# Kernel optimization log

Hardware: AMD Instinct MI355X
Metric: run time of the kernel (lower is better)

## Reference

```python
import jax, jax.numpy as jnp
import numpy as np

N, D, C, S = 100000, 512, 4096, 50000


def setup_inputs() -> dict:
    key = jax.random.key(0)
    k1, k2 = jax.random.split(key)
    X = jax.random.normal(k1, (N, D), dtype=jnp.float32)
    codebook_sum = jax.random.normal(k2, (C, D), dtype=jnp.float32)
    prompt_mask = jnp.arange(N) < S  # first S rows are support (True), rest are queries
    return {"X": X, "codebook_sum": codebook_sum, "prompt_mask": prompt_mask, "num_support": S}


def reference(X, codebook_sum, prompt_mask, num_support):
    # num_support is a static Python int (replaces torch.nonzero(prompt_mask) dynamic split)
    s = num_support
    support = X[:s]                                   # [S, D] support (prompt_mask==True)
    query = X[s:]                                     # [Q, D] queries (prompt_mask==False)
    # dense similarity matmul + top-1 nearest-codebook search + gather
    cos_sim = jnp.einsum('sd,cd->sc', support, codebook_sum)  # [S, C]
    top_idx = jnp.argmax(cos_sim, axis=1)             # [S]
    code_n = codebook_sum[top_idx]                    # [S, D] gathered nearest codes
    # mean-pooled prototypes broadcast over queries
    proto = jnp.mean(support, axis=0)                 # [D]
    proto_code = jnp.mean(code_n, axis=0)             # [D]
    # euclidean distances to each prototype
    query_score = jnp.sqrt(jnp.sum((query - proto) ** 2, axis=1))        # [Q]
    query_score_code = jnp.sqrt(jnp.sum((query - proto_code) ** 2, axis=1))  # [Q]
    return (query_score + query_score_code) / 2
```

## Files before the change

### kernel.cpp

```cpp
#include <hip/hip_runtime.h>
#include <hip/hip_bf16.h>

#define NTOT 100000
#define DIM  512
#define CB   4096
#define SSUP 50000
#define NQ   (NTOT - SSUP)

#define MTILES 391
#define MPAD   (MTILES * 128)
#define NTILES 32
#define NWG    (MTILES * NTILES)
#define CPX    (NWG / 8)

typedef __bf16 bf16x8 __attribute__((ext_vector_type(8)));
typedef __bf16 bf16x4 __attribute__((ext_vector_type(4)));
typedef float  f32x4  __attribute__((ext_vector_type(4)));

#define OFF_CBBF   0
#define OFF_XB     4194304
#define OFF_PV     55443456
#define OFF_PI     61849600
#define OFF_PSUM   68255744
#define OFF_PCSUM  68257792
#define OFF_HIST   68259840
#define OFF_TIDX   68276224
#define WS_NEED    (68276224 + 200000)
#define ZERO_BYTES (2048 + 2048 + 16384)

#define F_OFF_PSUM   4194304
#define F_OFF_PCSUM  4196352
#define F_OFF_HIST   4198400
#define F_OFF_TIDX   4214784

__device__ __forceinline__ void load_lds16(const void* g, void* l) {
    __builtin_amdgcn_global_load_lds(
        (const __attribute__((address_space(1))) void*)g,
        (__attribute__((address_space(3))) void*)l, 16, 0, 0);
}

#define BARRIER() __builtin_amdgcn_s_barrier()
#define VMC(N)    asm volatile("s_waitcnt vmcnt(" #N ")" ::: "memory")

__global__ void k_convert(const float* __restrict__ src, __bf16* __restrict__ dst) {
    int i = (blockIdx.x * 256 + threadIdx.x) * 4;
    float4 v = *(const float4*)(src + i);
    bf16x4 o;
    o[0] = (__bf16)v.x; o[1] = (__bf16)v.y; o[2] = (__bf16)v.z; o[3] = (__bf16)v.w;
    *(bf16x4*)(dst + i) = o;
}

__global__ __launch_bounds__(256)
void k_conv_psum(const float* __restrict__ X, __bf16* __restrict__ Xb,
                 float* __restrict__ protoSum)
{
    __shared__ float red[4][512];
    const int tid  = threadIdx.x;
    const int c8   = (tid & 63) * 8;
    const int rsub = tid >> 6;
    const size_t rbase = (size_t)blockIdx.x * 128 + rsub;

    float acc[8];
    #pragma unroll
    for (int j = 0; j < 8; ++j) acc[j] = 0.f;

    for (int r = 0; r < 128; r += 4) {
        const size_t row = rbase + r;
        const float* p = X + row * DIM + c8;
        float4 v0 = *(const float4*)p;
        float4 v1 = *(const float4*)(p + 4);
        bf16x8 o;
        o[0] = (__bf16)v0.x; o[1] = (__bf16)v0.y; o[2] = (__bf16)v0.z; o[3] = (__bf16)v0.w;
        o[4] = (__bf16)v1.x; o[5] = (__bf16)v1.y; o[6] = (__bf16)v1.z; o[7] = (__bf16)v1.w;
        *(bf16x8*)(Xb + row * DIM + c8) = o;
        if (row < SSUP) {
            acc[0] += v0.x; acc[1] += v0.y; acc[2] += v0.z; acc[3] += v0.w;
            acc[4] += v1.x; acc[5] += v1.y; acc[6] += v1.z; acc[7] += v1.w;
        }
    }
    #pragma unroll
    for (int j = 0; j < 8; ++j) red[rsub][c8 + j] = acc[j];
    __syncthreads();
    if (rsub == 0) {
        #pragma unroll
        for (int j = 0; j < 8; ++j)
            atomicAdd(&protoSum[c8 + j],
                      red[0][c8 + j] + red[1][c8 + j] + red[2][c8 + j] + red[3][c8 + j]);
    }
}


template<int MH, int NH>
__device__ __forceinline__ void mfma_quad_dummy() {}

__global__ __launch_bounds__(256, 2)
void k_gemm128(const __bf16* __restrict__ Xb, const __bf16* __restrict__ cbb,
               float* __restrict__ pv, int* __restrict__ pi)
{
    __shared__ __align__(16) char lds[65536];
    __shared__ float sv[128][2];
    __shared__ int   si[128][2];

    const int tid  = threadIdx.x;
    const int lane = tid & 63;
    const int wid  = tid >> 6;
    const int wm   = wid >> 1;
    const int wn   = wid & 1;
    const int l15  = lane & 15;
    const int q    = lane >> 4;

    const int lin = blockIdx.y * NTILES + blockIdx.x;
    const int swz = (lin & 7) * CPX + (lin >> 3);
    const int mt  = swz >> 5;
    const int nt  = swz & 31;
    const size_t r0  = (size_t)mt * 128;
    const size_t c0g = (size_t)nt * 128;

    const int off0 = l15 * 128 + ((q)     ^ (l15 & 7)) * 16;
    const int off1 = l15 * 128 + ((4 + q) ^ (l15 & 7)) * 16;

    const int ck0 = tid, ck1 = 256 + tid;
    const int rw0 = ck0 >> 3, rw1 = ck1 >> 3;
    const int sc0 = (ck0 & 7) ^ (rw0 & 7);
    const int sc1 = (ck1 & 7) ^ (rw1 & 7);
    const __bf16* pA0 = Xb  + (r0  + rw0) * DIM + sc0 * 8;
    const __bf16* pA1 = Xb  + (r0  + rw1) * DIM + sc1 * 8;
    const __bf16* pB0 = cbb + (c0g + rw0) * DIM + sc0 * 8;
    const __bf16* pB1 = cbb + (c0g + rw1) * DIM + sc1 * 8;
    const int d0 = ck0 * 16, d1 = ck1 * 16;
    const size_t HROW = (size_t)64 * DIM;

    f32x4 acc[4][4];
    #pragma unroll
    for (int i = 0; i < 4; ++i)
        #pragma unroll
        for (int j = 0; j < 4; ++j)
            acc[i][j] = (f32x4){0.f, 0.f, 0.f, 0.f};

    auto STAGE = [&](int bufo, int kt) {
        const int ko = kt * 64;
        char* lb = lds + bufo;
        load_lds16(pA0 + ko,        lb + d0);
        load_lds16(pA1 + ko,        lb + d1);
        load_lds16(pA0 + HROW + ko, lb + 8192 + d0);
        load_lds16(pA1 + HROW + ko, lb + 8192 + d1);
        load_lds16(pB0 + ko,        lb + 16384 + d0);
        load_lds16(pB1 + ko,        lb + 16384 + d1);
        load_lds16(pB0 + HROW + ko, lb + 24576 + d0);
        load_lds16(pB1 + HROW + ko, lb + 24576 + d1);
    };

    auto COMPUTE = [&](int bufo) {
        const char* ap = lds + bufo + wm * 8192;
        const char* bp = lds + bufo + 16384 + wn * 8192;
        bf16x8 a[4][2], b[4][2];
        #pragma unroll
        for (int m = 0; m < 4; ++m) {
            a[m][0] = *(const bf16x8*)(ap + m * 2048 + off0);
            a[m][1] = *(const bf16x8*)(ap + m * 2048 + off1);
        }
        #pragma unroll
        for (int n = 0; n < 4; ++n) {
            b[n][0] = *(const bf16x8*)(bp + n * 2048 + off0);
            b[n][1] = *(const bf16x8*)(bp + n * 2048 + off1);
        }
        __builtin_amdgcn_s_setprio(1);
        #pragma unroll
        for (int m = 0; m < 4; ++m)
            #pragma unroll
            for (int n = 0; n < 4; ++n)
                #pragma unroll
                for (int ks = 0; ks < 2; ++ks)
                    acc[m][n] = __builtin_amdgcn_mfma_f32_16x16x32_bf16(
                        a[m][ks], b[n][ks], acc[m][n], 0, 0, 0);
        __builtin_amdgcn_s_setprio(0);
    };

    STAGE(0, 0);
    STAGE(32768, 1);
    VMC(8);
    BARRIER();

    #pragma unroll
    for (int t = 0; t < 6; t += 2) {
        COMPUTE(0);
        BARRIER();
        STAGE(0, t + 2);
        VMC(8);
        BARRIER();
        COMPUTE(32768);
        BARRIER();
        STAGE(32768, t + 3);
        VMC(8);
        BARRIER();
    }

    COMPUTE(0);
    BARRIER();
    VMC(0);
    BARRIER();
    COMPUTE(32768);

    #pragma unroll
    for (int fm = 0; fm < 4; ++fm) {
        #pragma unroll
        for (int reg = 0; reg < 4; ++reg) {
            float v = -3.0e38f; int idx = 0;
            #pragma unroll
            for (int fn = 0; fn < 4; ++fn) {
                float x = acc[fm][fn][reg];
                int   c = (int)c0g + wn * 64 + fn * 16 + l15;
                if (x > v) { v = x; idx = c; }
            }
            #pragma unroll
            for (int off = 1; off < 16; off <<= 1) {
                float ov = __shfl_xor(v, off, 64);
                int   oi = __shfl_xor(idx, off, 64);
                if (ov > v) { v = ov; idx = oi; }
            }
            if (l15 == 0) {
                int rl = wm * 64 + fm * 16 + q * 4 + reg;
                sv[rl][wn] = v;
                si[rl][wn] = idx;
            }
        }
    }
    __syncthreads();
    if (tid < 128) {
        float v0 = sv[tid][0], v1 = sv[tid][1];
        size_t r = r0 + tid;
        pv[r * 32 + nt] = fmaxf(v0, v1);
        pi[r * 32 + nt] = (v1 > v0) ? si[tid][1] : si[tid][0];
    }
}

__global__ __launch_bounds__(256)
void k_reduce_hist(const float* __restrict__ pv, const int* __restrict__ pi,
                   int* __restrict__ hist) {
    __shared__ int lh[CB];
    const int tid = threadIdx.x;
    for (int i = tid; i < CB; i += 256) lh[i] = 0;
    __syncthreads();
    const int r = blockIdx.x * 256 + tid;
    if (r < SSUP) {
        float v = -3.0e38f; int idx = 0;
        #pragma unroll 8
        for (int j = 0; j < 32; ++j) {
            float x = pv[(size_t)r * 32 + j];
            if (x > v) { v = x; idx = pi[(size_t)r * 32 + j]; }
        }
        atomicAdd(&lh[idx], 1);
    }
    __syncthreads();
    for (int i = tid; i < CB; i += 256) {
        int v = lh[i];
        if (v) atomicAdd(&hist[i], v);
    }
}

__global__ void k_proto_sum(const float* __restrict__ X, float* __restrict__ protoSum) {
    const int d = threadIdx.x;
    const int r0 = blockIdx.x * 500;
    float acc = 0.f;
    for (int r = r0; r < r0 + 500; ++r)
        acc += X[(size_t)r * DIM + d];
    atomicAdd(&protoSum[d], acc);
}

__global__ __launch_bounds__(256, 2)
void k_gemm_argmax(const float* __restrict__ X, const __bf16* __restrict__ cbb,
                   int* __restrict__ top_idx)
{
    __shared__ float redv[64][2];
    __shared__ int   redi[64][2];

    const int tid  = threadIdx.x;
    const int wave = tid >> 6;
    const int lane = tid & 63;
    const int wm   = wave >> 1;
    const int wn   = wave & 1;
    const int l15  = lane & 15;
    const int q    = lane >> 4;
    const int r0   = blockIdx.x * 64;

    bf16x8 aflat[2][16];
    #pragma unroll
    for (int tm = 0; tm < 2; ++tm) {
        const int r = r0 + wm * 32 + tm * 16 + l15;
        const bool valid = (r < SSUP);
        const float* xr = X + (size_t)r * DIM + q * 8;
        #pragma unroll
        for (int kt = 0; kt < 16; ++kt) {
            float4 v0, v1;
            if (valid) {
                v0 = *(const float4*)(xr + kt * 32);
                v1 = *(const float4*)(xr + kt * 32 + 4);
            } else {
                v0 = make_float4(0.f, 0.f, 0.f, 0.f);
                v1 = v0;
            }
            bf16x8 f;
            f[0] = (__bf16)v0.x; f[1] = (__bf16)v0.y; f[2] = (__bf16)v0.z; f[3] = (__bf16)v0.w;
            f[4] = (__bf16)v1.x; f[5] = (__bf16)v1.y; f[6] = (__bf16)v1.z; f[7] = (__bf16)v1.w;
            aflat[tm][kt] = f;
        }
    }

    float mx[8];
    int   mi[8];
    #pragma unroll
    for (int i = 0; i < 8; ++i) { mx[i] = -3.0e38f; mi[i] = 0; }
    const f32x4 zero4 = {0.f, 0.f, 0.f, 0.f};

    for (int ct = 0; ct < 32; ++ct) {
        const int c0 = ct * 128 + wn * 64;
        const __bf16* bptr[4];
        #pragma unroll
        for (int tn = 0; tn < 4; ++tn)
            bptr[tn] = cbb + (size_t)(c0 + tn * 16 + l15) * DIM + q * 8;

        f32x4 acc[2][4];
        #pragma unroll
        for (int i = 0; i < 2; ++i)
            #pragma unroll
            for (int j = 0; j < 4; ++j)
                acc[i][j] = zero4;

        #pragma unroll
        for (int kt = 0; kt < 16; ++kt) {
            bf16x8 b[4];
            #pragma unroll
            for (int tn = 0; tn < 4; ++tn)
                b[tn] = *(const bf16x8*)(bptr[tn] + kt * 32);
            #pragma unroll
            for (int tm = 0; tm < 2; ++tm)
                #pragma unroll
                for (int tn = 0; tn < 4; ++tn)
                    acc[tm][tn] = __builtin_amdgcn_mfma_f32_16x16x32_bf16(
                        aflat[tm][kt], b[tn], acc[tm][tn], 0, 0, 0);
        }
        #pragma unroll
        for (int tm = 0; tm < 2; ++tm)
            #pragma unroll
            for (int tn = 0; tn < 4; ++tn)
                #pragma unroll
                for (int reg = 0; reg < 4; ++reg) {
                    float v = acc[tm][tn][reg];
                    int slot = tm * 4 + reg;
                    int col  = c0 + tn * 16 + l15;
                    if (v > mx[slot]) { mx[slot] = v; mi[slot] = col; }
                }
    }

    #pragma unroll
    for (int slot = 0; slot < 8; ++slot) {
        float v  = mx[slot];
        int  idx = mi[slot];
        #pragma unroll
        for (int off = 1; off < 16; off <<= 1) {
            float ov = __shfl_xor(v, off, 64);
            int   oi = __shfl_xor(idx, off, 64);
            if (ov > v) { v = ov; idx = oi; }
        }
        if (l15 == 0) {
            int rowl = wm * 32 + (slot >> 2) * 16 + q * 4 + (slot & 3);
            redv[rowl][wn] = v;
            redi[rowl][wn] = idx;
        }
    }
    __syncthreads();
    if (tid < 64) {
        int r = r0 + tid;
        if (r < SSUP) {
            float v0 = redv[tid][0], v1 = redv[tid][1];
            top_idx[r] = (v1 > v0) ? redi[tid][1] : redi[tid][0];
        }
    }
}

__global__ void k_hist(const int* __restrict__ top_idx, int* __restrict__ hist) {
    __shared__ int lh[CB];
    for (int i = threadIdx.x; i < CB; i += blockDim.x) lh[i] = 0;
    __syncthreads();
    for (int i = blockIdx.x * blockDim.x + threadIdx.x; i < SSUP; i += gridDim.x * blockDim.x)
        atomicAdd(&lh[top_idx[i]], 1);
    __syncthreads();
    for (int i = threadIdx.x; i < CB; i += blockDim.x) {
        int v = lh[i];
        if (v) atomicAdd(&hist[i], v);
    }
}

__global__ void k_proto_code(const float* __restrict__ cb, const int* __restrict__ hist,
                             float* __restrict__ pcSum) {
    const int d  = threadIdx.x;
    const int c0 = blockIdx.x * 64;
    float acc = 0.f;
    for (int c = c0; c < c0 + 64; ++c) {
        float w = (float)hist[c];
        if (w != 0.f) acc += w * cb[(size_t)c * DIM + d];
    }
    atomicAdd(&pcSum[d], acc);
}

__global__ void k_query(const float* __restrict__ X, const float* __restrict__ protoSum,
                        const float* __restrict__ pcSum, float* __restrict__ out) {
    const int lane   = threadIdx.x & 63;
    const int waveId = (blockIdx.x * blockDim.x + threadIdx.x) >> 6;
    const int nwaves = (gridDim.x * blockDim.x) >> 6;
    const float invS = 1.0f / (float)SSUP;

    for (int r = waveId; r < NQ; r += nwaves) {
        const float* xr = X + (size_t)(SSUP + r) * DIM;
        float s1 = 0.f, s2 = 0.f;
        #pragma unroll
        for (int i = 0; i < 2; ++i) {
            int dd = lane * 4 + i * 256;
            float4 xq = *(const float4*)(xr + dd);
            float4 p  = *(const float4*)(protoSum + dd);
            float4 pc = *(const float4*)(pcSum + dd);
            float d0, d1, d2, d3;
            d0 = xq.x - p.x * invS; d1 = xq.y - p.y * invS;
            d2 = xq.z - p.z * invS; d3 = xq.w - p.w * invS;
            s1 += d0 * d0 + d1 * d1 + d2 * d2 + d3 * d3;
            d0 = xq.x - pc.x * invS; d1 = xq.y - pc.y * invS;
            d2 = xq.z - pc.z * invS; d3 = xq.w - pc.w * invS;
            s2 += d0 * d0 + d1 * d1 + d2 * d2 + d3 * d3;
        }
        #pragma unroll
        for (int off = 32; off > 0; off >>= 1) {
            s1 += __shfl_xor(s1, off, 64);
            s2 += __shfl_xor(s2, off, 64);
        }
        if (lane == 0)
            out[r] = 0.5f * (sqrtf(s1) + sqrtf(s2));
    }
}

extern "C" void kernel_launch(void* const* d_in, const int* in_sizes, int n_in,
                              void* d_out, int out_size, void* d_ws, size_t ws_size,
                              hipStream_t stream) {
    const float* X  = (const float*)d_in[0];
    const float* cb = (const float*)d_in[1];
    float* out = (float*)d_out;
    char* ws = (char*)d_ws;

    __bf16* cbb = (__bf16*)(ws + OFF_CBBF);

    if (ws_size >= (size_t)WS_NEED) {
        __bf16* Xb       = (__bf16*)(ws + OFF_XB);
        float*  pv       = (float*)(ws + OFF_PV);
        int*    pi       = (int*)(ws + OFF_PI);
        float*  protoSum = (float*)(ws + OFF_PSUM);
        float*  pcSum    = (float*)(ws + OFF_PCSUM);
        int*    hist     = (int*)(ws + OFF_HIST);

        hipMemsetAsync(ws + OFF_PSUM, 0, ZERO_BYTES, stream);

        k_convert<<<(CB * DIM) / 1024, 256, 0, stream>>>(cb, cbb);
        k_conv_psum<<<MPAD / 128, 256, 0, stream>>>(X, Xb, protoSum);

        dim3 grid(NTILES, MTILES);
        k_gemm128<<<grid, 256, 0, stream>>>(Xb, cbb, pv, pi);

        k_reduce_hist<<<(SSUP + 255) / 256, 256, 0, stream>>>(pv, pi, hist);
        k_proto_code<<<CB / 64, 512, 0, stream>>>(cb, hist, pcSum);
        k_query<<<1024, 256, 0, stream>>>(X, protoSum, pcSum, out);
    } else {
        float*  protoSum = (float*)(ws + F_OFF_PSUM);
        float*  pcSum    = (float*)(ws + F_OFF_PCSUM);
        int*    hist     = (int*)(ws + F_OFF_HIST);
        int*    top_idx  = (int*)(ws + F_OFF_TIDX);

        hipMemsetAsync(ws + F_OFF_PSUM, 0, ZERO_BYTES, stream);

        k_convert<<<(CB * DIM) / 1024, 256, 0, stream>>>(cb, cbb);
        k_proto_sum<<<100, 512, 0, stream>>>(X, protoSum);
        k_gemm_argmax<<<(SSUP + 63) / 64, 256, 0, stream>>>(X, cbb, top_idx);
        k_hist<<<64, 256, 0, stream>>>(top_idx, hist);
        k_proto_code<<<CB / 64, 512, 0, stream>>>(cb, hist, pcSum);
        k_query<<<1024, 256, 0, stream>>>(X, protoSum, pcSum, out);
    }
}
```

Baseline: 681.3 us.

## Keep X tile in registers as bf16 and stream codebook through triple-buffered LDS

The GEMM kernel now loads each block's 64 rows of fp32 X directly from global memory, converts them to bf16 in registers, and keeps them resident for the whole K dimension. The codebook is streamed through a three-buffer LDS pipeline over half of all 4096 codes, with a running argmax kept in registers. This removes the separate X-to-bf16 conversion pass and its workspace write and re-read, and shrinks the partial argmax output from 32 slices to 2, so the reduce kernel reads less. The cost is heavy register pressure from holding A fragments, only 1564 blocks of smaller 64-row tiles, and codebook re-reads per block. The psum kernel now reads only support rows.

```diff
diff --git a/kernel.cpp b/kernel.cpp
--- a/kernel.cpp
+++ b/kernel.cpp
@@ -7,11 +7,10 @@
 #define SSUP 50000
 #define NQ   (NTOT - SSUP)
 
-#define MTILES 391
-#define MPAD   (MTILES * 128)
-#define NTILES 32
-#define NWG    (MTILES * NTILES)
-#define CPX    (NWG / 8)
+#define MB64   782
+#define MPAD   (MB64 * 64)
+#define NHALF  2
+#define NSTEPS 128
 
 typedef __bf16 bf16x8 __attribute__((ext_vector_type(8)));
 typedef __bf16 bf16x4 __attribute__((ext_vector_type(4)));
@@ -51,8 +50,7 @@
 }
 
 __global__ __launch_bounds__(256)
-void k_conv_psum(const float* __restrict__ X, __bf16* __restrict__ Xb,
-                 float* __restrict__ protoSum)
+void k_psum(const float* __restrict__ X, float* __restrict__ protoSum)
 {
     __shared__ float red[4][512];
     const int tid  = threadIdx.x;
@@ -66,14 +64,10 @@
 
     for (int r = 0; r < 128; r += 4) {
         const size_t row = rbase + r;
-        const float* p = X + row * DIM + c8;
-        float4 v0 = *(const float4*)p;
-        float4 v1 = *(const float4*)(p + 4);
-        bf16x8 o;
-        o[0] = (__bf16)v0.x; o[1] = (__bf16)v0.y; o[2] = (__bf16)v0.z; o[3] = (__bf16)v0.w;
-        o[4] = (__bf16)v1.x; o[5] = (__bf16)v1.y; o[6] = (__bf16)v1.z; o[7] = (__bf16)v1.w;
-        *(bf16x8*)(Xb + row * DIM + c8) = o;
         if (row < SSUP) {
+            const float* p = X + row * DIM + c8;
+            float4 v0 = *(const float4*)p;
+            float4 v1 = *(const float4*)(p + 4);
             acc[0] += v0.x; acc[1] += v0.y; acc[2] += v0.z; acc[3] += v0.w;
             acc[4] += v1.x; acc[5] += v1.y; acc[6] += v1.z; acc[7] += v1.w;
         }
@@ -89,17 +83,13 @@
     }
 }
 
-
-template<int MH, int NH>
-__device__ __forceinline__ void mfma_quad_dummy() {}
-
 __global__ __launch_bounds__(256, 2)
-void k_gemm128(const __bf16* __restrict__ Xb, const __bf16* __restrict__ cbb,
-               float* __restrict__ pv, int* __restrict__ pi)
+void k_gemm_areg(const float* __restrict__ X, const __bf16* __restrict__ cbb,
+                 float* __restrict__ pv, int* __restrict__ pi)
 {
-    __shared__ __align__(16) char lds[65536];
-    __shared__ float sv[128][2];
-    __shared__ int   si[128][2];
+    __shared__ __align__(16) char lds[49152];
+    __shared__ float sv[64][2];
+    __shared__ int   si[64][2];
 
     const int tid  = threadIdx.x;
     const int lane = tid & 63;
@@ -109,146 +99,143 @@
     const int l15  = lane & 15;
     const int q    = lane >> 4;
 
-    const int lin = blockIdx.y * NTILES + blockIdx.x;
-    const int swz = (lin & 7) * CPX + (lin >> 3);
-    const int mt  = swz >> 5;
-    const int nt  = swz & 31;
-    const size_t r0  = (size_t)mt * 128;
-    const size_t c0g = (size_t)nt * 128;
+    const int bm  = blockIdx.x >> 1;
+    const int nh  = blockIdx.x & 1;
+    const size_t r0 = (size_t)bm * 64;
+    const int ct0 = nh * 16;
+
+    bf16x8 aflat[2][16];
+    #pragma unroll
+    for (int tm = 0; tm < 2; ++tm) {
+        const size_t r = r0 + wm * 32 + tm * 16 + l15;
+        const float* xr = X + r * DIM + q * 8;
+        #pragma unroll
+        for (int kt = 0; kt < 16; ++kt) {
+            float4 v0 = *(const float4*)(xr + kt * 32);
+            float4 v1 = *(const float4*)(xr + kt * 32 + 4);
+            bf16x8 f;
+            f[0] = (__bf16)v0.x; f[1] = (__bf16)v0.y; f[2] = (__bf16)v0.z; f[3] = (__bf16)v0.w;
+            f[4] = (__bf16)v1.x; f[5] = (__bf16)v1.y; f[6] = (__bf16)v1.z; f[7] = (__bf16)v1.w;
+            aflat[tm][kt] = f;
+        }
+    }
+
+    const int sc   = (tid & 7) ^ ((tid >> 3) & 7);
+    const int pre0 = (tid >> 3) * DIM + sc * 8;
+
+    auto STAGE = [&](char* buf, int sp) {
+        const int c0s = (ct0 + (sp >> 3)) * 128;
+        const __bf16* base = cbb + (size_t)c0s * DIM + (sp & 7) * 64 + pre0;
+        #pragma unroll
+        for (int i = 0; i < 4; ++i)
+            load_lds16(base + i * 32 * DIM, buf + tid * 16 + i * 4096);
+    };
 
     const int off0 = l15 * 128 + ((q)     ^ (l15 & 7)) * 16;
     const int off1 = l15 * 128 + ((4 + q) ^ (l15 & 7)) * 16;
 
-    const int ck0 = tid, ck1 = 256 + tid;
-    const int rw0 = ck0 >> 3, rw1 = ck1 >> 3;
-    const int sc0 = (ck0 & 7) ^ (rw0 & 7);
-    const int sc1 = (ck1 & 7) ^ (rw1 & 7);
-    const __bf16* pA0 = Xb  + (r0  + rw0) * DIM + sc0 * 8;
-    const __bf16* pA1 = Xb  + (r0  + rw1) * DIM + sc1 * 8;
-    const __bf16* pB0 = cbb + (c0g + rw0) * DIM + sc0 * 8;
-    const __bf16* pB1 = cbb + (c0g + rw1) * DIM + sc1 * 8;
-    const int d0 = ck0 * 16, d1 = ck1 * 16;
-    const size_t HROW = (size_t)64 * DIM;
-
-    f32x4 acc[4][4];
-    #pragma unroll
-    for (int i = 0; i < 4; ++i)
-        #pragma unroll
-        for (int j = 0; j < 4; ++j)
-            acc[i][j] = (f32x4){0.f, 0.f, 0.f, 0.f};
-
-    auto STAGE = [&](int bufo, int kt) {
-        const int ko = kt * 64;
-        char* lb = lds + bufo;
-        load_lds16(pA0 + ko,        lb + d0);
-        load_lds16(pA1 + ko,        lb + d1);
-        load_lds16(pA0 + HROW + ko, lb + 8192 + d0);
-        load_lds16(pA1 + HROW + ko, lb + 8192 + d1);
-        load_lds16(pB0 + ko,        lb + 16384 + d0);
-        load_lds16(pB1 + ko,        lb + 16384 + d1);
-        load_lds16(pB0 + HROW + ko, lb + 24576 + d0);
-        load_lds16(pB1 + HROW + ko, lb + 24576 + d1);
-    };
-
-    auto COMPUTE = [&](int bufo) {
-        const char* ap = lds + bufo + wm * 8192;
-        const char* bp = lds + bufo + 16384 + wn * 8192;
-        bf16x8 a[4][2], b[4][2];
-        #pragma unroll
-        for (int m = 0; m < 4; ++m) {
-            a[m][0] = *(const bf16x8*)(ap + m * 2048 + off0);
-            a[m][1] = *(const bf16x8*)(ap + m * 2048 + off1);
-        }
-        #pragma unroll
-        for (int n = 0; n < 4; ++n) {
-            b[n][0] = *(const bf16x8*)(bp + n * 2048 + off0);
-            b[n][1] = *(const bf16x8*)(bp + n * 2048 + off1);
-        }
-        __builtin_amdgcn_s_setprio(1);
-        #pragma unroll
-        for (int m = 0; m < 4; ++m)
-            #pragma unroll
-            for (int n = 0; n < 4; ++n)
+    char* p0 = lds;
+    char* p1 = lds + 16384;
+    char* p2 = lds + 32768;
+
+    STAGE(p0, 0);
+    STAGE(p1, 1);
+
+    float mx[8]; int mi[8];
+    #pragma unroll
+    for (int i = 0; i < 8; ++i) { mx[i] = -3.0e38f; mi[i] = 0; }
+
+    int s = 0;
+    #pragma unroll 1
+    for (int ct = 0; ct < 16; ++ct) {
+        f32x4 acc[2][4];
+        #pragma unroll
+        for (int i = 0; i < 2; ++i)
+            #pragma unroll
+            for (int j = 0; j < 4; ++j)
+                acc[i][j] = (f32x4){0.f, 0.f, 0.f, 0.f};
+
+        #pragma unroll
+        for (int kb = 0; kb < 8; ++kb) {
+            VMC(4);
+            BARRIER();
+            {
+                int sp = s + 2; if (sp > NSTEPS - 1) sp = NSTEPS - 1;
+                STAGE(p2, sp);
+            }
+            const char* bp = p0 + wn * 8192;
+            bf16x8 b[4][2];
+            #pragma unroll
+            for (int tn = 0; tn < 4; ++tn) {
+                b[tn][0] = *(const bf16x8*)(bp + tn * 2048 + off0);
+                b[tn][1] = *(const bf16x8*)(bp + tn * 2048 + off1);
+            }
+            __builtin_amdgcn_s_setprio(1);
+            #pragma unroll
+            for (int tm = 0; tm < 2; ++tm)
                 #pragma unroll
-                for (int ks = 0; ks < 2; ++ks)
-                    acc[m][n] = __builtin_amdgcn_mfma_f32_16x16x32_bf16(
-                        a[m][ks], b[n][ks], acc[m][n], 0, 0, 0);
-        __builtin_amdgcn_s_setprio(0);
-    };
-
-    STAGE(0, 0);
-    STAGE(32768, 1);
-    VMC(8);
-    BARRIER();
-
-    #pragma unroll
-    for (int t = 0; t < 6; t += 2) {
-        COMPUTE(0);
-        BARRIER();
-        STAGE(0, t + 2);
-        VMC(8);
-        BARRIER();
-        COMPUTE(32768);
-        BARRIER();
-        STAGE(32768, t + 3);
-        VMC(8);
-        BARRIER();
-    }
-
-    COMPUTE(0);
-    BARRIER();
+                for (int tn = 0; tn < 4; ++tn)
+                    #pragma unroll
+                    for (int ks = 0; ks < 2; ++ks)
+                        acc[tm][tn] = __builtin_amdgcn_mfma_f32_16x16x32_bf16(
+                            aflat[tm][2 * kb + ks], b[tn][ks], acc[tm][tn], 0, 0, 0);
+            __builtin_amdgcn_s_setprio(0);
+            char* t = p0; p0 = p1; p1 = p2; p2 = t;
+            ++s;
+        }
+
+        const int cbase = (ct0 + ct) * 128 + wn * 64;
+        #pragma unroll
+        for (int tm = 0; tm < 2; ++tm)
+            #pragma unroll
+            for (int tn = 0; tn < 4; ++tn)
+                #pragma unroll
+                for (int reg = 0; reg < 4; ++reg) {
+                    float v = acc[tm][tn][reg];
+                    int slot = tm * 4 + reg;
+                    int col  = cbase + tn * 16 + l15;
+                    if (v > mx[slot]) { mx[slot] = v; mi[slot] = col; }
+                }
+    }
     VMC(0);
-    BARRIER();
-    COMPUTE(32768);
-
-    #pragma unroll
-    for (int fm = 0; fm < 4; ++fm) {
-        #pragma unroll
-        for (int reg = 0; reg < 4; ++reg) {
-            float v = -3.0e38f; int idx = 0;
-            #pragma unroll
-            for (int fn = 0; fn < 4; ++fn) {
-                float x = acc[fm][fn][reg];
-                int   c = (int)c0g + wn * 64 + fn * 16 + l15;
-                if (x > v) { v = x; idx = c; }
-            }
-            #pragma unroll
-            for (int off = 1; off < 16; off <<= 1) {
-                float ov = __shfl_xor(v, off, 64);
-                int   oi = __shfl_xor(idx, off, 64);
-                if (ov > v) { v = ov; idx = oi; }
-            }
-            if (l15 == 0) {
-                int rl = wm * 64 + fm * 16 + q * 4 + reg;
-                sv[rl][wn] = v;
-                si[rl][wn] = idx;
-            }
-        }
-    }
-    __syncthreads();
-    if (tid < 128) {
+
+    #pragma unroll
+    for (int slot = 0; slot < 8; ++slot) {
+        float v  = mx[slot];
+        int  idx = mi[slot];
+        #pragma unroll
+        for (int off = 1; off < 16; off <<= 1) {
+            float ov = __shfl_xor(v, off, 64);
+            int   oi = __shfl_xor(idx, off, 64);
+            if (ov > v) { v = ov; idx = oi; }
+        }
+        if (l15 == 0) {
+            int rowl = wm * 32 + (slot >> 2) * 16 + q * 4 + (slot & 3);
+            sv[rowl][wn] = v;
+            si[rowl][wn] = idx;
+        }
+    }
+    __syncthreads();
+    if (tid < 64) {
         float v0 = sv[tid][0], v1 = sv[tid][1];
         size_t r = r0 + tid;
-        pv[r * 32 + nt] = fmaxf(v0, v1);
-        pi[r * 32 + nt] = (v1 > v0) ? si[tid][1] : si[tid][0];
+        pv[r * 2 + nh] = fmaxf(v0, v1);
+        pi[r * 2 + nh] = (v1 > v0) ? si[tid][1] : si[tid][0];
     }
 }
 
 __global__ __launch_bounds__(256)
-void k_reduce_hist(const float* __restrict__ pv, const int* __restrict__ pi,
-                   int* __restrict__ hist) {
+void k_reduce_hist2(const float* __restrict__ pv, const int* __restrict__ pi,
+                    int* __restrict__ hist) {
     __shared__ int lh[CB];
     const int tid = threadIdx.x;
     for (int i = tid; i < CB; i += 256) lh[i] = 0;
     __syncthreads();
     const int r = blockIdx.x * 256 + tid;
     if (r < SSUP) {
-        float v = -3.0e38f; int idx = 0;
-        #pragma unroll 8
-        for (int j = 0; j < 32; ++j) {
-            float x = pv[(size_t)r * 32 + j];
-            if (x > v) { v = x; idx = pi[(size_t)r * 32 + j]; }
-        }
+        float v0 = pv[(size_t)r * 2];
+        float v1 = pv[(size_t)r * 2 + 1];
+        int idx = (v1 > v0) ? pi[(size_t)r * 2 + 1] : pi[(size_t)r * 2];
         atomicAdd(&lh[idx], 1);
     }
     __syncthreads();
@@ -448,7 +435,6 @@
     __bf16* cbb = (__bf16*)(ws + OFF_CBBF);
 
     if (ws_size >= (size_t)WS_NEED) {
-        __bf16* Xb       = (__bf16*)(ws + OFF_XB);
         float*  pv       = (float*)(ws + OFF_PV);
         int*    pi       = (int*)(ws + OFF_PI);
         float*  protoSum = (float*)(ws + OFF_PSUM);
@@ -458,12 +444,11 @@
         hipMemsetAsync(ws + OFF_PSUM, 0, ZERO_BYTES, stream);
 
         k_convert<<<(CB * DIM) / 1024, 256, 0, stream>>>(cb, cbb);
-        k_conv_psum<<<MPAD / 128, 256, 0, stream>>>(X, Xb, protoSum);
-
-        dim3 grid(NTILES, MTILES);
-        k_gemm128<<<grid, 256, 0, stream>>>(Xb, cbb, pv, pi);
-
-        k_reduce_hist<<<(SSUP + 255) / 256, 256, 0, stream>>>(pv, pi, hist);
+        k_psum<<<MPAD / 128, 256, 0, stream>>>(X, protoSum);
+
+        k_gemm_areg<<<MB64 * NHALF, 256, 0, stream>>>(X, cbb, pv, pi);
+
+        k_reduce_hist2<<<(SSUP + 255) / 256, 256, 0, stream>>>(pv, pi, hist);
         k_proto_code<<<CB / 64, 512, 0, stream>>>(cb, hist, pcSum);
         k_query<<<1024, 256, 0, stream>>>(X, protoSum, pcSum, out);
     } else {
```

New measurement: 626.2 us. 1.09x faster.
